# Optimization experiments

Hardware: AMD Instinct MI355X
Metric: run time of the kernel (lower is better)

Reference implementation:

```python
import jax, jax.numpy as jnp
import numpy as np

NUM_EXPERTS = 4
MLP_RATIO = 4


def setup_inputs() -> dict:
    key = jax.random.key(0)
    k1, k2, k3, k4, k5, k6 = jax.random.split(key, 6)
    B, N, D = 4, 4096, 1024
    OUT = 1024
    H = D * MLP_RATIO
    x = jax.random.normal(k1, (B, N, D), dtype=jnp.float32)
    expert_mask = jax.random.randint(k2, (B, N), 0, NUM_EXPERTS, dtype=jnp.int64)
    w1 = jax.random.normal(k3, (H, D), dtype=jnp.float32) * 0.02
    b1 = jax.random.normal(k4, (H,), dtype=jnp.float32) * 0.02
    w2 = jax.random.normal(k5, (OUT, H), dtype=jnp.float32) * 0.02
    b2 = jax.random.normal(k6, (OUT,), dtype=jnp.float32) * 0.02
    return {"x": x, "expert_mask": expert_mask, "w1": w1, "b1": b1, "w2": w2, "b2": b2}


def reference(x, expert_mask, w1, b1, w2, b2):
    # x: [B, N, D]; expert_mask: [B, N] in [0, NUM_EXPERTS)
    D = x.shape[-1]
    OUT = w2.shape[0]
    E = NUM_EXPERTS
    y = jnp.zeros(x.shape[:-1] + (OUT,), dtype=x.dtype)
    for e in range(E):
        shift = E - 1 - e  # expert E-1 uses full width
        d_in = D >> shift
        d_hid = d_in * MLP_RATIO
        d_out = OUT >> shift
        # nested slice of shared weights
        h = jax.nn.gelu(
            jnp.einsum('bnd,hd->bnh', x[..., :d_in], w1[:d_hid, :d_in]) + b1[:d_hid],
            approximate=False,
        )
        ye = jnp.einsum('bnh,oh->bno', h, w2[:d_out, :d_hid]) + b2[:d_out]
        ye = jnp.pad(ye, ((0, 0), (0, 0), (0, OUT - d_out)))  # zero-fill unused dims
        y = y + jnp.where((expert_mask == e)[..., None], ye, jnp.zeros((), dtype=x.dtype))
    return y
```

## Files before the change

### kernel.cpp

```cpp
#include <hip/hip_runtime.h>
#include <hip/hip_bf16.h>

#define T_TOK 16384
#define DMODEL 1024
#define HDIM 4096
#define OUTD 1024

typedef __attribute__((ext_vector_type(8))) short short8_t;
typedef __attribute__((ext_vector_type(4))) float f32x4;

#define WS_COUNTS_OFF 0
#define WS_HBASE_OFF 64
#define WS_XBASE_OFF 96
#define WS_LIST_OFF 128
#define WS_XC_OFF   ((size_t)1 << 20)
#define WS_W1BF_OFF ((size_t)34 << 20)
#define WS_W2BF_OFF ((size_t)43 << 20)
#define WS_HBUF_OFF ((size_t)52 << 20)

#define W1N (HDIM * DMODEL)
#define W2N (OUTD * HDIM)

__device__ __forceinline__ short f2bf(float f) {
    union { float f; unsigned u; } x; x.f = f;
    unsigned r = x.u + 0x7FFFu + ((x.u >> 16) & 1u);
    return (short)(r >> 16);
}

__device__ __forceinline__ float gelu_fast(float v) {
    float z = fabsf(v) * 0.7071067811865476f;
    float t = __builtin_amdgcn_rcpf(fmaf(0.3275911f, z, 1.0f));
    float poly = t * fmaf(t, fmaf(t, fmaf(t, fmaf(t, 1.061405429f, -1.453152027f),
                                          1.421413741f), -0.284496736f),
                          0.254829592f);
    float e = fmaf(-poly, __expf(-z * z), 1.0f);
    float erfv = copysignf(e, v);
    return 0.5f * v * (1.0f + erfv);
}

__device__ __forceinline__ void conv8(const float* __restrict__ s, short* __restrict__ d) {
    const float4* s4 = (const float4*)s;
    float4 f0 = s4[0], f1 = s4[1];
    short8_t v;
    v[0] = f2bf(f0.x); v[1] = f2bf(f0.y); v[2] = f2bf(f0.z); v[3] = f2bf(f0.w);
    v[4] = f2bf(f1.x); v[5] = f2bf(f1.y); v[6] = f2bf(f1.z); v[7] = f2bf(f1.w);
    *(short8_t*)d = v;
}

__device__ __forceinline__ void gl_lds16(const short* g, short* lds) {
    __builtin_amdgcn_global_load_lds(
        (const __attribute__((address_space(1))) void*)g,
        (__attribute__((address_space(3))) void*)lds, 16, 0, 0);
}

__global__ void k_convert(const float* __restrict__ w1, const float* __restrict__ w2,
                          short* __restrict__ w1bf, short* __restrict__ w2bf) {
    size_t elem = ((size_t)blockIdx.x * blockDim.x + threadIdx.x) * 8;
    if (elem < (size_t)W1N) {
        conv8(w1 + elem, w1bf + elem);
    } else {
        size_t o = elem - W1N; conv8(w2 + o, w2bf + o);
    }
}

__global__ void k_init(int* counts) {
    if (threadIdx.x < 4) counts[threadIdx.x] = 0;
}

__global__ void k_build(const int* __restrict__ mask, int* counts, int* list) {
    __shared__ int hcnt[4], hb[4], hpos[4];
    int tid = threadIdx.x;
    if (tid < 4) hcnt[tid] = 0;
    __syncthreads();
    int t = blockIdx.x * 256 + tid;
    int e = mask[t] & 3;
    atomicAdd(&hcnt[e], 1);
    __syncthreads();
    if (tid < 4) { hb[tid] = atomicAdd(&counts[tid], hcnt[tid]); hpos[tid] = 0; }
    __syncthreads();
    int p = atomicAdd(&hpos[e], 1);
    list[e * T_TOK + hb[e] + p] = t;
}

__global__ void k_bases(const int* counts, unsigned long long* hbase,
                        unsigned long long* xbase) {
    if (threadIdx.x == 0) {
        unsigned long long ha = 0, xa = 0;
        for (int e = 0; e < 4; ++e) {
            hbase[e] = ha; xbase[e] = xa;
            int d_in = 128 << e;
            ha += (unsigned long long)counts[e] * (unsigned long long)(d_in * 4);
            xa += (unsigned long long)counts[e] * (unsigned long long)d_in;
        }
    }
}

__global__ void k_xgather(const float* __restrict__ x, const int* __restrict__ counts,
                          const unsigned long long* __restrict__ xbase,
                          const int* __restrict__ list, short* __restrict__ xc) {
    const int e = blockIdx.y;
    const int d_in = 128 << e;
    const int cnt = counts[e];
    const size_t nel = (size_t)cnt * d_in;
    const int* lst = list + e * T_TOK;
    short* dst = xc + xbase[e];
    for (size_t idx = ((size_t)blockIdx.x * 256 + threadIdx.x) * 8; idx < nel;
         idx += (size_t)gridDim.x * 256 * 8) {
        int row = (int)(idx >> (7 + e));
        int col = (int)(idx & (d_in - 1));
        int tok = lst[row];
        conv8(x + (size_t)tok * DMODEL + col, dst + idx);
    }
}

__global__ void k_zfill(const int* __restrict__ counts, const int* __restrict__ list,
                        float* __restrict__ y) {
    const int e = blockIdx.y;
    const int d_out = 128 << e;
    const int cnt = counts[e];
    const int* lst = list + e * T_TOK;
    const int wv = threadIdx.x >> 6;
    const int lane = threadIdx.x & 63;
    for (int r = blockIdx.x * 4 + wv; r < cnt; r += gridDim.x * 4) {
        float* row = y + (size_t)lst[r] * OUTD;
        for (int c = d_out + lane * 4; c < OUTD; c += 256)
            *(float4*)(row + c) = (float4){0.f, 0.f, 0.f, 0.f};
    }
}

__global__ __launch_bounds__(256) void k_pass1(
    const short* __restrict__ xc, const short* __restrict__ w1bf,
    const float* __restrict__ b1,
    const int* __restrict__ counts, const unsigned long long* __restrict__ hbase,
    const unsigned long long* __restrict__ xbase, short* __restrict__ hbuf)
{
    int by = blockIdx.y;
    int e, nt;
    if (by < 32)      { e = 3; nt = by; }
    else if (by < 48) { e = 2; nt = by - 32; }
    else if (by < 56) { e = 1; nt = by - 48; }
    else              { e = 0; nt = by - 56; }
    const int d_in = 128 << e;
    const int d_hid = d_in * 4;
    const int n0 = nt * 128;
    const int cnt = counts[e];
    const unsigned long long hb = hbase[e];
    const short* xe = xc + xbase[e];

    __shared__ short Ab[64 * 64];
    __shared__ short Bb[128 * 64];

    const int tid = threadIdx.x;
    const int lane = tid & 63;
    const int w = tid >> 6;
    const int l3 = lane >> 3;
    const int ch = lane & 7;
    const int wm = (w & 1) * 32;
    const int wn = (w >> 1) * 64;

    for (int m0 = blockIdx.x * 64; m0 < cnt; m0 += 64 * 64) {
        int rA[2];
#pragma unroll
        for (int j = 0; j < 2; ++j) {
            int rr = m0 + j * 32 + w * 8 + l3;
            rA[j] = (rr >= cnt) ? (cnt - 1) : rr;
        }

        f32x4 acc[2][4];
#pragma unroll
        for (int i = 0; i < 2; ++i)
#pragma unroll
            for (int j = 0; j < 4; ++j)
                acc[i][j] = (f32x4){0.f, 0.f, 0.f, 0.f};

        for (int k0 = 0; k0 < d_in; k0 += 64) {
#pragma unroll
            for (int j = 0; j < 2; ++j) {
                int r = j * 32 + w * 8 + l3;
                gl_lds16(xe + (size_t)rA[j] * d_in + k0 + ((ch ^ (r & 7)) << 3),
                         &Ab[(j * 32 + w * 8) * 64]);
            }
#pragma unroll
            for (int j = 0; j < 4; ++j) {
                int r = j * 32 + w * 8 + l3;
                gl_lds16(w1bf + (size_t)(n0 + r) * DMODEL + k0 + ((ch ^ (r & 7)) << 3),
                         &Bb[(j * 32 + w * 8) * 64]);
            }
            __syncthreads();
#pragma unroll
            for (int kk = 0; kk < 2; ++kk) {
                short8_t af[2], bfr[4];
                const int q = (lane >> 4) + kk * 4;
#pragma unroll
                for (int mt = 0; mt < 2; ++mt) {
                    int row = wm + mt * 16 + (lane & 15);
                    af[mt] = *(const short8_t*)&Ab[((row << 3) | (q ^ (row & 7))) << 3];
                }
#pragma unroll
                for (int ntn = 0; ntn < 4; ++ntn) {
                    int row = wn + ntn * 16 + (lane & 15);
                    bfr[ntn] = *(const short8_t*)&Bb[((row << 3) | (q ^ (row & 7))) << 3];
                }
#pragma unroll
                for (int mt = 0; mt < 2; ++mt)
#pragma unroll
                    for (int ntn = 0; ntn < 4; ++ntn)
                        acc[mt][ntn] = __builtin_amdgcn_mfma_f32_16x16x32_bf16(
                            af[mt], bfr[ntn], acc[mt][ntn], 0, 0, 0);
            }
            __syncthreads();
        }

        const int cl = lane & 15;
        const int qr = lane >> 4;
#pragma unroll
        for (int ntn = 0; ntn < 4; ++ntn) {
            int col = n0 + wn + ntn * 16 + cl;
            float bias = b1[col];
#pragma unroll
            for (int mt = 0; mt < 2; ++mt) {
#pragma unroll
                for (int r = 0; r < 4; ++r) {
                    int row = wm + mt * 16 + qr * 4 + r;
                    if (m0 + row < cnt) {
                        float v = acc[mt][ntn][r] + bias;
                        hbuf[hb + (unsigned long long)(m0 + row) * d_hid + col] =
                            f2bf(gelu_fast(v));
                    }
                }
            }
        }
    }
}

__global__ __launch_bounds__(256) void k_pass2(
    const short* __restrict__ hbuf, const short* __restrict__ w2bf,
    const float* __restrict__ b2,
    const int* __restrict__ counts, const unsigned long long* __restrict__ hbase,
    const int* __restrict__ list, float* __restrict__ y)
{
    int by = blockIdx.y;
    int e, nt;
    if (by < 8)       { e = 3; nt = by; }
    else if (by < 12) { e = 2; nt = by - 8; }
    else if (by < 14) { e = 1; nt = by - 12; }
    else              { e = 0; nt = 0; }
    const int d_in = 128 << e;
    const int d_hid = d_in * 4;
    const int n0 = nt * 128;
    const int cnt = counts[e];
    const int* lst = list + e * T_TOK;
    const unsigned long long hb = hbase[e];

    __shared__ short Ab[2 * 64 * 64];
    __shared__ short Bb[2 * 128 * 64];

    const int tid = threadIdx.x;
    const int lane = tid & 63;
    const int w = tid >> 6;
    const int l3 = lane >> 3;
    const int ch = lane & 7;
    const int wm = (w & 1) * 32;
    const int wn = (w >> 1) * 64;

    for (int m0 = blockIdx.x * 64; m0 < cnt; m0 += 64 * 64) {
        int rA[2];
#pragma unroll
        for (int j = 0; j < 2; ++j) {
            int rr = m0 + j * 32 + w * 8 + l3;
            rA[j] = (rr >= cnt) ? (cnt - 1) : rr;
        }

        f32x4 acc[2][4];
#pragma unroll
        for (int i = 0; i < 2; ++i)
#pragma unroll
            for (int j = 0; j < 4; ++j)
                acc[i][j] = (f32x4){0.f, 0.f, 0.f, 0.f};

        const int ks = d_hid >> 6;
#pragma unroll
        for (int j = 0; j < 2; ++j) {
            int r = j * 32 + w * 8 + l3;
            gl_lds16(hbuf + hb + (size_t)rA[j] * d_hid + ((ch ^ (r & 7)) << 3),
                     &Ab[(j * 32 + w * 8) * 64]);
        }
#pragma unroll
        for (int j = 0; j < 4; ++j) {
            int r = j * 32 + w * 8 + l3;
            gl_lds16(w2bf + (size_t)(n0 + r) * HDIM + ((ch ^ (r & 7)) << 3),
                     &Bb[(j * 32 + w * 8) * 64]);
        }
        for (int kt = 0; kt < ks; ++kt) {
            const int p = kt & 1;
            __syncthreads();
            if (kt + 1 < ks) {
                const int kn = (kt + 1) << 6;
                const int qb = 1 - p;
#pragma unroll
                for (int j = 0; j < 2; ++j) {
                    int r = j * 32 + w * 8 + l3;
                    gl_lds16(hbuf + hb + (size_t)rA[j] * d_hid + kn + ((ch ^ (r & 7)) << 3),
                             &Ab[(qb * 4096) + (j * 32 + w * 8) * 64]);
                }
#pragma unroll
                for (int j = 0; j < 4; ++j) {
                    int r = j * 32 + w * 8 + l3;
                    gl_lds16(w2bf + (size_t)(n0 + r) * HDIM + kn + ((ch ^ (r & 7)) << 3),
                             &Bb[(qb * 8192) + (j * 32 + w * 8) * 64]);
                }
            }
            const short* Ap = &Ab[p * 4096];
            const short* Bp = &Bb[p * 8192];
#pragma unroll
            for (int kk = 0; kk < 2; ++kk) {
                short8_t af[2], bfr[4];
                const int q = (lane >> 4) + kk * 4;
#pragma unroll
                for (int mt = 0; mt < 2; ++mt) {
                    int row = wm + mt * 16 + (lane & 15);
                    af[mt] = *(const short8_t*)&Ap[((row << 3) | (q ^ (row & 7))) << 3];
                }
#pragma unroll
                for (int ntn = 0; ntn < 4; ++ntn) {
                    int row = wn + ntn * 16 + (lane & 15);
                    bfr[ntn] = *(const short8_t*)&Bp[((row << 3) | (q ^ (row & 7))) << 3];
                }
#pragma unroll
                for (int mt = 0; mt < 2; ++mt)
#pragma unroll
                    for (int ntn = 0; ntn < 4; ++ntn)
                        acc[mt][ntn] = __builtin_amdgcn_mfma_f32_16x16x32_bf16(
                            af[mt], bfr[ntn], acc[mt][ntn], 0, 0, 0);
            }
        }
        __syncthreads();

        const int cl = lane & 15;
        const int qr = lane >> 4;
#pragma unroll
        for (int ntn = 0; ntn < 4; ++ntn) {
            int col = n0 + wn + ntn * 16 + cl;
            float bias = b2[col];
#pragma unroll
            for (int mt = 0; mt < 2; ++mt) {
#pragma unroll
                for (int r = 0; r < 4; ++r) {
                    int row = wm + mt * 16 + qr * 4 + r;
                    if (m0 + row < cnt) {
                        int tok = lst[m0 + row];
                        y[(size_t)tok * OUTD + col] = acc[mt][ntn][r] + bias;
                    }
                }
            }
        }
    }
}

extern "C" void kernel_launch(void* const* d_in, const int* in_sizes, int n_in,
                              void* d_out, int out_size, void* d_ws, size_t ws_size,
                              hipStream_t stream) {
    const float* x  = (const float*)d_in[0];
    const int* mask = (const int*)d_in[1];
    const float* w1 = (const float*)d_in[2];
    const float* b1 = (const float*)d_in[3];
    const float* w2 = (const float*)d_in[4];
    const float* b2 = (const float*)d_in[5];
    float* y = (float*)d_out;

    char* ws = (char*)d_ws;
    int* counts = (int*)(ws + WS_COUNTS_OFF);
    unsigned long long* hbase = (unsigned long long*)(ws + WS_HBASE_OFF);
    unsigned long long* xbase = (unsigned long long*)(ws + WS_XBASE_OFF);
    int* list = (int*)(ws + WS_LIST_OFF);
    short* xc   = (short*)(ws + WS_XC_OFF);
    short* w1bf = (short*)(ws + WS_W1BF_OFF);
    short* w2bf = (short*)(ws + WS_W2BF_OFF);
    short* hbuf = (short*)(ws + WS_HBUF_OFF);

    k_convert<<<(W1N + W2N) / 8 / 256, 256, 0, stream>>>(w1, w2, w1bf, w2bf);

    k_init<<<1, 64, 0, stream>>>(counts);
    k_build<<<T_TOK / 256, 256, 0, stream>>>(mask, counts, list);
    k_bases<<<1, 1, 0, stream>>>(counts, hbase, xbase);
    k_xgather<<<dim3(128, 4), 256, 0, stream>>>(x, counts, xbase, list, xc);

    k_zfill<<<dim3(256, 3), 256, 0, stream>>>(counts, list, y);

    k_pass1<<<dim3(64, 60), 256, 0, stream>>>(xc, w1bf, b1, counts, hbase, xbase, hbuf);
    k_pass2<<<dim3(64, 15), 256, 0, stream>>>(hbuf, w2bf, b2, counts, hbase, list, y);
}
```

Measured before the change: 377.1 us.

## Merge setup kernels and load GEMM fragments directly from global memory

The counter init is folded into the weight conversion kernel, the bases kernel is replaced by per-block prefix computation, and the gather and zero-fill kernels become one launch, cutting the launch count from eight to five. Both GEMM passes drop LDS staging and barriers and instead load MFMA fragments straight from global memory into registers, with a two-stage register double buffer. This removes synchronisation and LDS traffic but loses data reuse across waves, so global and L2 traffic rises and loads are less coalesced.

```diff
diff --git a/kernel.cpp b/kernel.cpp
--- a/kernel.cpp
+++ b/kernel.cpp
@@ -10,8 +10,6 @@
 typedef __attribute__((ext_vector_type(4))) float f32x4;
 
 #define WS_COUNTS_OFF 0
-#define WS_HBASE_OFF 64
-#define WS_XBASE_OFF 96
 #define WS_LIST_OFF 128
 #define WS_XC_OFF   ((size_t)1 << 20)
 #define WS_W1BF_OFF ((size_t)34 << 20)
@@ -47,24 +45,29 @@
     *(short8_t*)d = v;
 }
 
-__device__ __forceinline__ void gl_lds16(const short* g, short* lds) {
-    __builtin_amdgcn_global_load_lds(
-        (const __attribute__((address_space(1))) void*)g,
-        (__attribute__((address_space(3))) void*)lds, 16, 0, 0);
+__device__ __forceinline__ void bases_for(const int* __restrict__ counts, int e,
+                                          unsigned long long* hb,
+                                          unsigned long long* xb) {
+    unsigned long long h = 0, x = 0;
+    for (int i = 0; i < e; ++i) {
+        unsigned long long c = (unsigned long long)counts[i];
+        int din = 128 << i;
+        x += c * (unsigned long long)din;
+        h += c * (unsigned long long)(din * 4);
+    }
+    *hb = h; *xb = x;
 }
 
 __global__ void k_convert(const float* __restrict__ w1, const float* __restrict__ w2,
-                          short* __restrict__ w1bf, short* __restrict__ w2bf) {
+                          short* __restrict__ w1bf, short* __restrict__ w2bf,
+                          int* counts) {
+    if (blockIdx.x == 0 && threadIdx.x < 4) counts[threadIdx.x] = 0;
     size_t elem = ((size_t)blockIdx.x * blockDim.x + threadIdx.x) * 8;
     if (elem < (size_t)W1N) {
         conv8(w1 + elem, w1bf + elem);
     } else {
         size_t o = elem - W1N; conv8(w2 + o, w2bf + o);
     }
-}
-
-__global__ void k_init(int* counts) {
-    if (threadIdx.x < 4) counts[threadIdx.x] = 0;
 }
 
 __global__ void k_build(const int* __restrict__ mask, int* counts, int* list) {
@@ -82,57 +85,44 @@
     list[e * T_TOK + hb[e] + p] = t;
 }
 
-__global__ void k_bases(const int* counts, unsigned long long* hbase,
-                        unsigned long long* xbase) {
-    if (threadIdx.x == 0) {
-        unsigned long long ha = 0, xa = 0;
-        for (int e = 0; e < 4; ++e) {
-            hbase[e] = ha; xbase[e] = xa;
-            int d_in = 128 << e;
-            ha += (unsigned long long)counts[e] * (unsigned long long)(d_in * 4);
-            xa += (unsigned long long)counts[e] * (unsigned long long)d_in;
-        }
-    }
-}
-
 __global__ void k_xgather(const float* __restrict__ x, const int* __restrict__ counts,
-                          const unsigned long long* __restrict__ xbase,
-                          const int* __restrict__ list, short* __restrict__ xc) {
-    const int e = blockIdx.y;
-    const int d_in = 128 << e;
-    const int cnt = counts[e];
-    const size_t nel = (size_t)cnt * d_in;
-    const int* lst = list + e * T_TOK;
-    short* dst = xc + xbase[e];
-    for (size_t idx = ((size_t)blockIdx.x * 256 + threadIdx.x) * 8; idx < nel;
-         idx += (size_t)gridDim.x * 256 * 8) {
-        int row = (int)(idx >> (7 + e));
-        int col = (int)(idx & (d_in - 1));
-        int tok = lst[row];
-        conv8(x + (size_t)tok * DMODEL + col, dst + idx);
-    }
-}
-
-__global__ void k_zfill(const int* __restrict__ counts, const int* __restrict__ list,
-                        float* __restrict__ y) {
-    const int e = blockIdx.y;
-    const int d_out = 128 << e;
-    const int cnt = counts[e];
-    const int* lst = list + e * T_TOK;
-    const int wv = threadIdx.x >> 6;
-    const int lane = threadIdx.x & 63;
-    for (int r = blockIdx.x * 4 + wv; r < cnt; r += gridDim.x * 4) {
-        float* row = y + (size_t)lst[r] * OUTD;
-        for (int c = d_out + lane * 4; c < OUTD; c += 256)
-            *(float4*)(row + c) = (float4){0.f, 0.f, 0.f, 0.f};
+                          const int* __restrict__ list, short* __restrict__ xc,
+                          float* __restrict__ y) {
+    if (blockIdx.y < 4) {
+        const int e = blockIdx.y;
+        const int d_in = 128 << e;
+        const int cnt = counts[e];
+        unsigned long long hbD, xb;
+        bases_for(counts, e, &hbD, &xb);
+        const size_t nel = (size_t)cnt * d_in;
+        const int* lst = list + e * T_TOK;
+        short* dst = xc + xb;
+        for (size_t idx = ((size_t)blockIdx.x * 256 + threadIdx.x) * 8; idx < nel;
+             idx += (size_t)gridDim.x * 256 * 8) {
+            int row = (int)(idx >> (7 + e));
+            int col = (int)(idx & (d_in - 1));
+            int tok = lst[row];
+            conv8(x + (size_t)tok * DMODEL + col, dst + idx);
+        }
+    } else {
+        const int e = blockIdx.y - 4;
+        const int d_out = 128 << e;
+        const int cnt = counts[e];
+        const int* lst = list + e * T_TOK;
+        const int wv = threadIdx.x >> 6;
+        const int lane = threadIdx.x & 63;
+        for (int r = blockIdx.x * 4 + wv; r < cnt; r += gridDim.x * 4) {
+            float* row = y + (size_t)lst[r] * OUTD;
+            for (int c = d_out + lane * 4; c < OUTD; c += 256)
+                *(float4*)(row + c) = (float4){0.f, 0.f, 0.f, 0.f};
+        }
     }
 }
 
 __global__ __launch_bounds__(256) void k_pass1(
     const short* __restrict__ xc, const short* __restrict__ w1bf,
-    const float* __restrict__ b1,
-    const int* __restrict__ counts, const unsigned long long* __restrict__ hbase,
-    const unsigned long long* __restrict__ xbase, short* __restrict__ hbuf)
+    const float* __restrict__ b1, const int* __restrict__ counts,
+    short* __restrict__ hbuf)
 {
     int by = blockIdx.y;
     int e, nt;
@@ -144,26 +134,30 @@
     const int d_hid = d_in * 4;
     const int n0 = nt * 128;
     const int cnt = counts[e];
-    const unsigned long long hb = hbase[e];
-    const short* xe = xc + xbase[e];
-
-    __shared__ short Ab[64 * 64];
-    __shared__ short Bb[128 * 64];
+    unsigned long long hb, xb;
+    bases_for(counts, e, &hb, &xb);
+    const short* xe = xc + xb;
 
     const int tid = threadIdx.x;
     const int lane = tid & 63;
     const int w = tid >> 6;
-    const int l3 = lane >> 3;
-    const int ch = lane & 7;
     const int wm = (w & 1) * 32;
     const int wn = (w >> 1) * 64;
+    const int kq = (lane >> 4) * 8;
+    const int rl = lane & 15;
+
+    const short* pb[4];
+#pragma unroll
+    for (int nn = 0; nn < 4; ++nn)
+        pb[nn] = w1bf + (size_t)(n0 + wn + nn * 16 + rl) * DMODEL + kq;
 
     for (int m0 = blockIdx.x * 64; m0 < cnt; m0 += 64 * 64) {
-        int rA[2];
-#pragma unroll
-        for (int j = 0; j < 2; ++j) {
-            int rr = m0 + j * 32 + w * 8 + l3;
-            rA[j] = (rr >= cnt) ? (cnt - 1) : rr;
+        const short* pa[2];
+#pragma unroll
+        for (int mt = 0; mt < 2; ++mt) {
+            int rr = m0 + wm + mt * 16 + rl;
+            rr = (rr >= cnt) ? (cnt - 1) : rr;
+            pa[mt] = xe + (size_t)rr * d_in + kq;
         }
 
         f32x4 acc[2][4];
@@ -173,43 +167,28 @@
             for (int j = 0; j < 4; ++j)
                 acc[i][j] = (f32x4){0.f, 0.f, 0.f, 0.f};
 
-        for (int k0 = 0; k0 < d_in; k0 += 64) {
-#pragma unroll
-            for (int j = 0; j < 2; ++j) {
-                int r = j * 32 + w * 8 + l3;
-                gl_lds16(xe + (size_t)rA[j] * d_in + k0 + ((ch ^ (r & 7)) << 3),
-                         &Ab[(j * 32 + w * 8) * 64]);
-            }
-#pragma unroll
-            for (int j = 0; j < 4; ++j) {
-                int r = j * 32 + w * 8 + l3;
-                gl_lds16(w1bf + (size_t)(n0 + r) * DMODEL + k0 + ((ch ^ (r & 7)) << 3),
-                         &Bb[(j * 32 + w * 8) * 64]);
-            }
-            __syncthreads();
-#pragma unroll
-            for (int kk = 0; kk < 2; ++kk) {
-                short8_t af[2], bfr[4];
-                const int q = (lane >> 4) + kk * 4;
-#pragma unroll
-                for (int mt = 0; mt < 2; ++mt) {
-                    int row = wm + mt * 16 + (lane & 15);
-                    af[mt] = *(const short8_t*)&Ab[((row << 3) | (q ^ (row & 7))) << 3];
-                }
-#pragma unroll
-                for (int ntn = 0; ntn < 4; ++ntn) {
-                    int row = wn + ntn * 16 + (lane & 15);
-                    bfr[ntn] = *(const short8_t*)&Bb[((row << 3) | (q ^ (row & 7))) << 3];
-                }
-#pragma unroll
-                for (int mt = 0; mt < 2; ++mt)
-#pragma unroll
-                    for (int ntn = 0; ntn < 4; ++ntn)
-                        acc[mt][ntn] = __builtin_amdgcn_mfma_f32_16x16x32_bf16(
-                            af[mt], bfr[ntn], acc[mt][ntn], 0, 0, 0);
-            }
-            __syncthreads();
-        }
+        short8_t aX[2], bX[4], aY[2], bY[4];
+#define LDF1(A, B, koff) do {                                              \
+        _Pragma("unroll") for (int i = 0; i < 2; ++i)                      \
+            A[i] = *(const short8_t*)(pa[i] + (koff));                     \
+        _Pragma("unroll") for (int i = 0; i < 4; ++i)                      \
+            B[i] = *(const short8_t*)(pb[i] + (koff)); } while (0)
+#define MM1(A, B) do {                                                     \
+        _Pragma("unroll") for (int mt = 0; mt < 2; ++mt)                   \
+        _Pragma("unroll") for (int nn = 0; nn < 4; ++nn)                   \
+            acc[mt][nn] = __builtin_amdgcn_mfma_f32_16x16x32_bf16(         \
+                A[mt], B[nn], acc[mt][nn], 0, 0, 0); } while (0)
+
+        LDF1(aX, bX, 0);
+        LDF1(aY, bY, 32);
+        for (int k = 0; k < d_in; k += 64) {
+            MM1(aX, bX);
+            if (k + 64 < d_in) LDF1(aX, bX, k + 64);
+            MM1(aY, bY);
+            if (k + 96 < d_in) LDF1(aY, bY, k + 96);
+        }
+#undef LDF1
+#undef MM1
 
         const int cl = lane & 15;
         const int qr = lane >> 4;
@@ -235,8 +214,7 @@
 
 __global__ __launch_bounds__(256) void k_pass2(
     const short* __restrict__ hbuf, const short* __restrict__ w2bf,
-    const float* __restrict__ b2,
-    const int* __restrict__ counts, const unsigned long long* __restrict__ hbase,
+    const float* __restrict__ b2, const int* __restrict__ counts,
     const int* __restrict__ list, float* __restrict__ y)
 {
     int by = blockIdx.y;
@@ -250,25 +228,29 @@
     const int n0 = nt * 128;
     const int cnt = counts[e];
     const int* lst = list + e * T_TOK;
-    const unsigned long long hb = hbase[e];
-
-    __shared__ short Ab[2 * 64 * 64];
-    __shared__ short Bb[2 * 128 * 64];
+    unsigned long long hb, xb;
+    bases_for(counts, e, &hb, &xb);
 
     const int tid = threadIdx.x;
     const int lane = tid & 63;
     const int w = tid >> 6;
-    const int l3 = lane >> 3;
-    const int ch = lane & 7;
     const int wm = (w & 1) * 32;
     const int wn = (w >> 1) * 64;
+    const int kq = (lane >> 4) * 8;
+    const int rl = lane & 15;
+
+    const short* pb[4];
+#pragma unroll
+    for (int nn = 0; nn < 4; ++nn)
+        pb[nn] = w2bf + (size_t)(n0 + wn + nn * 16 + rl) * HDIM + kq;
 
     for (int m0 = blockIdx.x * 64; m0 < cnt; m0 += 64 * 64) {
-        int rA[2];
-#pragma unroll
-        for (int j = 0; j < 2; ++j) {
-            int rr = m0 + j * 32 + w * 8 + l3;
-            rA[j] = (rr >= cnt) ? (cnt - 1) : rr;
+        const short* pa[2];
+#pragma unroll
+        for (int mt = 0; mt < 2; ++mt) {
+            int rr = m0 + wm + mt * 16 + rl;
+            rr = (rr >= cnt) ? (cnt - 1) : rr;
+            pa[mt] = hbuf + hb + (size_t)rr * d_hid + kq;
         }
 
         f32x4 acc[2][4];
@@ -278,63 +260,28 @@
             for (int j = 0; j < 4; ++j)
                 acc[i][j] = (f32x4){0.f, 0.f, 0.f, 0.f};
 
-        const int ks = d_hid >> 6;
-#pragma unroll
-        for (int j = 0; j < 2; ++j) {
-            int r = j * 32 + w * 8 + l3;
-            gl_lds16(hbuf + hb + (size_t)rA[j] * d_hid + ((ch ^ (r & 7)) << 3),
-                     &Ab[(j * 32 + w * 8) * 64]);
-        }
-#pragma unroll
-        for (int j = 0; j < 4; ++j) {
-            int r = j * 32 + w * 8 + l3;
-            gl_lds16(w2bf + (size_t)(n0 + r) * HDIM + ((ch ^ (r & 7)) << 3),
-                     &Bb[(j * 32 + w * 8) * 64]);
-        }
-        for (int kt = 0; kt < ks; ++kt) {
-            const int p = kt & 1;
-            __syncthreads();
-            if (kt + 1 < ks) {
-                const int kn = (kt + 1) << 6;
-                const int qb = 1 - p;
-#pragma unroll
-                for (int j = 0; j < 2; ++j) {
-                    int r = j * 32 + w * 8 + l3;
-                    gl_lds16(hbuf + hb + (size_t)rA[j] * d_hid + kn + ((ch ^ (r & 7)) << 3),
-                             &Ab[(qb * 4096) + (j * 32 + w * 8) * 64]);
-                }
-#pragma unroll
-                for (int j = 0; j < 4; ++j) {
-                    int r = j * 32 + w * 8 + l3;
-                    gl_lds16(w2bf + (size_t)(n0 + r) * HDIM + kn + ((ch ^ (r & 7)) << 3),
-                             &Bb[(qb * 8192) + (j * 32 + w * 8) * 64]);
-                }
-            }
-            const short* Ap = &Ab[p * 4096];
-            const short* Bp = &Bb[p * 8192];
-#pragma unroll
-            for (int kk = 0; kk < 2; ++kk) {
-                short8_t af[2], bfr[4];
-                const int q = (lane >> 4) + kk * 4;
-#pragma unroll
-                for (int mt = 0; mt < 2; ++mt) {
-                    int row = wm + mt * 16 + (lane & 15);
-                    af[mt] = *(const short8_t*)&Ap[((row << 3) | (q ^ (row & 7))) << 3];
-                }
-#pragma unroll
-                for (int ntn = 0; ntn < 4; ++ntn) {
-                    int row = wn + ntn * 16 + (lane & 15);
-                    bfr[ntn] = *(const short8_t*)&Bp[((row << 3) | (q ^ (row & 7))) << 3];
-                }
-#pragma unroll
-                for (int mt = 0; mt < 2; ++mt)
-#pragma unroll
-                    for (int ntn = 0; ntn < 4; ++ntn)
-                        acc[mt][ntn] = __builtin_amdgcn_mfma_f32_16x16x32_bf16(
-                            af[mt], bfr[ntn], acc[mt][ntn], 0, 0, 0);
-            }
-        }
-        __syncthreads();
+        short8_t aX[2], bX[4], aY[2], bY[4];
+#define LDF2(A, B, koff) do {                                              \
+        _Pragma("unroll") for (int i = 0; i < 2; ++i)                      \
+            A[i] = *(const short8_t*)(pa[i] + (koff));                     \
+        _Pragma("unroll") for (int i = 0; i < 4; ++i)                      \
+            B[i] = *(const short8_t*)(pb[i] + (koff)); } while (0)
+#define MM2(A, B) do {                                                     \
+        _Pragma("unroll") for (int mt = 0; mt < 2; ++mt)                   \
+        _Pragma("unroll") for (int nn = 0; nn < 4; ++nn)                   \
+            acc[mt][nn] = __builtin_amdgcn_mfma_f32_16x16x32_bf16(         \
+                A[mt], B[nn], acc[mt][nn], 0, 0, 0); } while (0)
+
+        LDF2(aX, bX, 0);
+        LDF2(aY, bY, 32);
+        for (int k = 0; k < d_hid; k += 64) {
+            MM2(aX, bX);
+            if (k + 64 < d_hid) LDF2(aX, bX, k + 64);
+            MM2(aY, bY);
+            if (k + 96 < d_hid) LDF2(aY, bY, k + 96);
+        }
+#undef LDF2
+#undef MM2
 
         const int cl = lane & 15;
         const int qr = lane >> 4;
@@ -370,23 +317,15 @@
 
     char* ws = (char*)d_ws;
     int* counts = (int*)(ws + WS_COUNTS_OFF);
-    unsigned long long* hbase = (unsigned long long*)(ws + WS_HBASE_OFF);
-    unsigned long long* xbase = (unsigned long long*)(ws + WS_XBASE_OFF);
     int* list = (int*)(ws + WS_LIST_OFF);
     short* xc   = (short*)(ws + WS_XC_OFF);
     short* w1bf = (short*)(ws + WS_W1BF_OFF);
     short* w2bf = (short*)(ws + WS_W2BF_OFF);
     short* hbuf = (short*)(ws + WS_HBUF_OFF);
 
-    k_convert<<<(W1N + W2N) / 8 / 256, 256, 0, stream>>>(w1, w2, w1bf, w2bf);
-
-    k_init<<<1, 64, 0, stream>>>(counts);
+    k_convert<<<(W1N + W2N) / 8 / 256, 256, 0, stream>>>(w1, w2, w1bf, w2bf, counts);
     k_build<<<T_TOK / 256, 256, 0, stream>>>(mask, counts, list);
-    k_bases<<<1, 1, 0, stream>>>(counts, hbase, xbase);
-    k_xgather<<<dim3(128, 4), 256, 0, stream>>>(x, counts, xbase, list, xc);
-
-    k_zfill<<<dim3(256, 3), 256, 0, stream>>>(counts, list, y);
-
-    k_pass1<<<dim3(64, 60), 256, 0, stream>>>(xc, w1bf, b1, counts, hbase, xbase, hbuf);
-    k_pass2<<<dim3(64, 15), 256, 0, stream>>>(hbuf, w2bf, b2, counts, hbase, list, y);
-}
+    k_xgather<<<dim3(128, 7), 256, 0, stream>>>(x, counts, list, xc, y);
+    k_pass1<<<dim3(64, 60), 256, 0, stream>>>(xc, w1bf, b1, counts, hbuf);
+    k_pass2<<<dim3(64, 15), 256, 0, stream>>>(hbuf, w2bf, b2, counts, list, y);
+}
```

Measured after the change: 787.3 us. 109% more time.
